# Kernel tuning notes

Measured on AMD Instinct MI355X. Metric: run time of the kernel, lower is better.

Reference implementation:

```python
import jax, jax.numpy as jnp
import numpy as np

GAMMA = 0.3
R_PERCENT = 0.2
LAMBDA_PENALTY = 0.5
EPS = 1e-06

B_SZ, N_HEADS, K_FULL = 16, 32, 32768
K_IMG = 16384


def _zscore(x):
    mu = x.mean(axis=-1, keepdims=True)
    std = jnp.sqrt(((x - mu) ** 2).mean(axis=-1, keepdims=True))  # unbiased=False
    return (x - mu) / (std + EPS)


def _topk_binary(scores, k):
    # scores: [B,H] -> binary mask [B,H]; only strictly-positive topk values count
    vals, idx = jax.lax.top_k(scores, k)
    b = jnp.arange(scores.shape[0])[:, None]
    return jnp.zeros_like(scores).at[b, idx].set((vals > 0).astype(scores.dtype))


def setup_inputs() -> dict:
    key = jax.random.key(0)
    k1, k2, k3, k4, k5 = jax.random.split(key, 5)
    attn_logits_last = jax.random.normal(k1, (B_SZ, N_HEADS, K_FULL), dtype=jnp.float32)
    # exactly K_IMG image tokens per row (alternating pattern -> strided gather)
    image_mask = jnp.tile((jnp.arange(K_FULL) % 2 == 0).astype(jnp.int32)[None, :], (B_SZ, 1))
    feat_C = jax.random.normal(k2, (B_SZ, K_IMG), dtype=jnp.float32)
    feat_A = jax.random.normal(k3, (B_SZ, K_IMG), dtype=jnp.float32)
    feat_D = jax.random.normal(k4, (B_SZ, K_IMG), dtype=jnp.float32)
    feat_B = jax.random.normal(k5, (B_SZ, K_IMG), dtype=jnp.float32)
    return {"attn_logits_last": attn_logits_last, "image_mask": image_mask,
            "feat_C": feat_C, "feat_A": feat_A, "feat_D": feat_D, "feat_B": feat_B}


def reference(attn_logits_last, image_mask, feat_C, feat_A, feat_D, feat_B):
    B, H, K_full = attn_logits_last.shape
    K_img = feat_C.shape[1]

    # --- compute_rf ---
    C_t = jax.nn.relu(_zscore(feat_C))
    A_t = jax.nn.sigmoid(_zscore(feat_A))
    D_t = jax.nn.sigmoid(_zscore(feat_D))
    B_t = jax.nn.sigmoid(_zscore(feat_B))
    denom = jnp.maximum(1.0 + LAMBDA_PENALTY * (D_t + B_t), EPS)
    rf = jnp.maximum(C_t * A_t / denom, 0.0)  # [B,K_img]

    # --- align: positions of image tokens (exactly K_img ones per row) ---
    idx = jax.vmap(lambda m: jnp.nonzero(m, size=K_img)[0])(image_mask)  # [B,K_img]

    # --- image-normalized attention ---
    probs_full = jax.nn.softmax(attn_logits_last, axis=-1)
    mask_f = image_mask[:, None, :].astype(attn_logits_last.dtype)  # [B,1,K_full]
    probs_img = probs_full * mask_f
    probs_img_norm = probs_img / jnp.maximum(probs_img.sum(axis=-1, keepdims=True), EPS)
    attn_img_norm = jnp.take_along_axis(probs_img_norm, idx[:, None, :], axis=-1)  # [B,H,K_img]

    # --- dynamic head roles ---
    low_rf = jnp.maximum(1.0 - rf, 0.0)
    s_pos = (attn_img_norm * rf[:, None, :]).sum(axis=-1)   # [B,H]
    s_neg = (attn_img_norm * low_rf[:, None, :]).sum(axis=-1)
    k_heads = min(max(1, int(np.ceil(R_PERCENT * H))), H)
    m_pos = _topk_binary(s_pos, k_heads)
    neg_scores = jnp.where(m_pos > 0, -jnp.inf, s_neg)
    m_neg = _topk_binary(neg_scores, k_heads) * (m_pos == 0).astype(s_pos.dtype)

    # --- delta and scatter back to full logits ---
    delta_img = GAMMA * (m_pos[:, :, None] * rf[:, None, :]
                         - m_neg[:, :, None] * low_rf[:, None, :])  # [B,H,K_img]
    delta_full = jax.vmap(
        lambda d, i: jnp.zeros((H, K_full), attn_logits_last.dtype).at[:, i].set(d)
    )(delta_img, idx)
    delta_full = delta_full * mask_f
    return attn_logits_last + delta_full
```

## Files before the change

kernel.cpp:

```cpp
#include <hip/hip_runtime.h>
#include <math.h>

#define GAMMA 0.3f
#define EPS 1e-6f
#define B_SZ 16
#define NH 32
#define KF 32768
#define KI 16384
#define KHEADS 7

constexpr int OFF_MU    = 0;
constexpr int OFF_SD    = 64;
constexpr int OFF_RAWS  = 128;
constexpr int OFF_RAWP  = 640;
constexpr int OFF_RAWN  = 1152;
constexpr int IOFF_BSUM = 1664;
constexpr int OFF_RF    = 4096;
constexpr int OFF_RFF   = OFF_RF + B_SZ * KI;

__global__ __launch_bounds__(256) void k_stats_cnt(const float* __restrict__ fC,
        const float* __restrict__ fA, const float* __restrict__ fD,
        const float* __restrict__ fB, const int* __restrict__ mask,
        float* __restrict__ ws) {
    __shared__ double r1[256], r2[256];
    __shared__ int sred[256];
    int bid = blockIdx.x, t = threadIdx.x;
    if (bid < 64) {
        int b = bid >> 2, f = bid & 3;
        const float* src;
        if (f == 0) src = fC; else if (f == 1) src = fA; else if (f == 2) src = fD; else src = fB;
        src += (size_t)b * KI;
        double s = 0.0, s2 = 0.0;
        for (int i = t; i < KI / 4; i += 256) {
            float4 v = ((const float4*)src)[i];
            s  += (double)v.x + (double)v.y + (double)v.z + (double)v.w;
            s2 += (double)v.x * v.x + (double)v.y * v.y + (double)v.z * v.z + (double)v.w * v.w;
        }
        r1[t] = s; r2[t] = s2; __syncthreads();
        for (int off = 128; off > 0; off >>= 1) {
            if (t < off) { r1[t] += r1[t + off]; r2[t] += r2[t + off]; }
            __syncthreads();
        }
        if (t == 0) {
            double mu  = r1[0] * (1.0 / KI);
            double var = fmax(r2[0] * (1.0 / KI) - mu * mu, 0.0);
            ws[OFF_MU + bid] = (float)mu;
            ws[OFF_SD + bid] = (float)(sqrt(var) + (double)EPS);
        }
    } else {
        int cblk = bid - 64;
        if (cblk < 6) ws[OFF_RAWS + cblk * 256 + t] = 0.f;
        const int* mrow = mask + (size_t)cblk * 2048;
        int4 m0 = *(const int4*)(mrow + t * 8);
        int4 m1 = *(const int4*)(mrow + t * 8 + 4);
        int cnt = (m0.x != 0) + (m0.y != 0) + (m0.z != 0) + (m0.w != 0)
                + (m1.x != 0) + (m1.y != 0) + (m1.z != 0) + (m1.w != 0);
        sred[t] = cnt; __syncthreads();
        for (int off = 128; off > 0; off >>= 1) {
            if (t < off) sred[t] += sred[t + off];
            __syncthreads();
        }
        if (t == 0) ((int*)ws)[IOFF_BSUM + cblk] = sred[0];
    }
}

__global__ __launch_bounds__(256) void k_rf(const float* __restrict__ fC,
        const float* __restrict__ fA, const float* __restrict__ fD,
        const float* __restrict__ fB, float* __restrict__ ws) {
    int blk = blockIdx.x, t = threadIdx.x;
    int base = blk * 1024 + t * 4;
    int b = base >> 14;
    const float* mu = ws + OFF_MU + b * 4;
    const float* sd = ws + OFF_SD + b * 4;
    float4 vC = *(const float4*)(fC + base);
    float4 vA = *(const float4*)(fA + base);
    float4 vD = *(const float4*)(fD + base);
    float4 vB = *(const float4*)(fB + base);
    float rf4[4];
    float c4[4] = {vC.x, vC.y, vC.z, vC.w};
    float a4[4] = {vA.x, vA.y, vA.z, vA.w};
    float d4[4] = {vD.x, vD.y, vD.z, vD.w};
    float b4[4] = {vB.x, vB.y, vB.z, vB.w};
    #pragma unroll
    for (int j = 0; j < 4; ++j) {
        float Ct = fmaxf((c4[j] - mu[0]) / sd[0], 0.f);
        float At = 1.f / (1.f + __expf(-((a4[j] - mu[1]) / sd[1])));
        float Dt = 1.f / (1.f + __expf(-((d4[j] - mu[2]) / sd[2])));
        float Bt = 1.f / (1.f + __expf(-((b4[j] - mu[3]) / sd[3])));
        float denom = fmaxf(1.f + 0.5f * (Dt + Bt), EPS);
        rf4[j] = fmaxf(Ct * At / denom, 0.f);
    }
    *(float4*)(ws + OFF_RF + base) = *(float4*)rf4;
}

__global__ __launch_bounds__(256) void k_expand(const int* __restrict__ mask,
                                                float* __restrict__ ws) {
    int blk = blockIdx.x, t = threadIdx.x;
    int b = blk >> 4, c = blk & 15;
    const int* bsum = (const int*)ws + IOFF_BSUM;
    int boff = 0;
    for (int i = 0; i < c; ++i) boff += bsum[(b << 4) + i];
    const int* mrow = mask + (size_t)blk * 2048;
    int4 m0 = *(const int4*)(mrow + t * 8);
    int4 m1 = *(const int4*)(mrow + t * 8 + 4);
    int mv[8] = {m0.x, m0.y, m0.z, m0.w, m1.x, m1.y, m1.z, m1.w};
    int cnt = 0;
    #pragma unroll
    for (int j = 0; j < 8; ++j) cnt += (mv[j] != 0);
    __shared__ int sc[256];
    sc[t] = cnt; __syncthreads();
    for (int off = 1; off < 256; off <<= 1) {
        int v = (t >= off) ? sc[t - off] : 0;
        __syncthreads();
        sc[t] += v;
        __syncthreads();
    }
    int r = boff + sc[t] - cnt;
    const float* rf = ws + OFF_RF + b * KI;
    float vr[8];
    #pragma unroll
    for (int j = 0; j < 8; ++j) {
        if (mv[j]) { vr[j] = rf[r]; ++r; }
        else       { vr[j] = -1.f; }
    }
    float* rff = ws + OFF_RFF + (size_t)blk * 2048 + t * 8;
    *(float4*)(rff)     = *(float4*)(vr);
    *(float4*)(rff + 4) = *(float4*)(vr + 4);
}

__global__ __launch_bounds__(256) void k_scores(const float* __restrict__ attn,
                                                float* __restrict__ ws) {
    int g = blockIdx.x, t = threadIdx.x;
    int bh = g >> 1, half = g & 1;
    int b = bh >> 5;
    const float* xr  = attn + ((size_t)bh << 15) + ((size_t)half << 14);
    const float* rff = ws + OFF_RFF + ((size_t)b << 15) + ((size_t)half << 14);
    float S = 0.f, P = 0.f, N = 0.f;
    #pragma unroll 4
    for (int i = 0; i < 16; ++i) {
        int k = (i * 256 + t) * 4;
        float4 xs = *(const float4*)(xr + k);
        float4 rv = *(const float4*)(rff + k);
        float xa[4] = {xs.x, xs.y, xs.z, xs.w};
        float va[4] = {rv.x, rv.y, rv.z, rv.w};
        #pragma unroll
        for (int j = 0; j < 4; ++j) {
            float e = __expf(xa[j]);
            bool on = va[j] >= 0.f;
            float rfv  = fmaxf(va[j], 0.f);
            float lrfv = on ? fmaxf(1.f - va[j], 0.f) : 0.f;
            S += on ? e : 0.f;
            P = fmaf(e, rfv, P);
            N = fmaf(e, lrfv, N);
        }
    }
    __shared__ float rs[256], rp[256], rn[256];
    rs[t] = S; rp[t] = P; rn[t] = N;
    __syncthreads();
    for (int off = 128; off > 0; off >>= 1) {
        if (t < off) { rs[t] += rs[t + off]; rp[t] += rp[t + off]; rn[t] += rn[t + off]; }
        __syncthreads();
    }
    if (t == 0) {
        atomicAdd(&ws[OFF_RAWS + bh], rs[0]);
        atomicAdd(&ws[OFF_RAWP + bh], rp[0]);
        atomicAdd(&ws[OFF_RAWN + bh], rn[0]);
    }
}

__global__ __launch_bounds__(256) void k_out(const float* __restrict__ attn,
        const float* __restrict__ ws, float* __restrict__ out) {
    unsigned int t = threadIdx.x;
    unsigned int flat = (blockIdx.x * 256 + t) * 4;
    unsigned int bh = flat >> 15;
    unsigned int b  = bh >> 5;
    unsigned int h  = bh & 31;

    __shared__ float ssp[NH], snv[NH];
    __shared__ int smp[NH];
    __shared__ float s_gp, s_gn;
    if (t < NH) {
        float S0 = ws[OFF_RAWS + b * NH + t];
        ssp[t] = ws[OFF_RAWP + b * NH + t] / S0;
        snv[t] = ws[OFF_RAWN + b * NH + t] / S0;
    }
    __syncthreads();
    if (t < NH) {
        float sp = ssp[t];
        int cnt = 0;
        for (int j = 0; j < NH; ++j) { float o = ssp[j]; cnt += (o > sp) || (o == sp && (int)j < (int)t); }
        smp[t] = (cnt < KHEADS) && (sp > 0.f);
    }
    __syncthreads();
    if (t < NH && smp[t]) snv[t] = -INFINITY;
    __syncthreads();
    if (t == 0) {
        float gp = 0.f, gn = 0.f;
        if (smp[h]) gp = GAMMA;
        else {
            float nv = snv[h];
            int cnt = 0;
            for (int j = 0; j < NH; ++j) { float o = snv[j]; cnt += (o > nv) || (o == nv && j < (int)h); }
            if ((cnt < KHEADS) && (nv > 0.f)) gn = GAMMA;
        }
        s_gp = gp; s_gn = gn;
    }
    __syncthreads();

    float gp = s_gp, gn = s_gn;
    const float* rff = ws + OFF_RFF + ((size_t)b << 15);
    unsigned int k = flat & (KF - 1);
    float4 xs = *(const float4*)(attn + flat);
    float4 rv = *(const float4*)(rff + k);
    float va[4] = {rv.x, rv.y, rv.z, rv.w};
    float xa[4] = {xs.x, xs.y, xs.z, xs.w};
    float oa[4];
    #pragma unroll
    for (int j = 0; j < 4; ++j) {
        bool on = va[j] >= 0.f;
        float rfv  = fmaxf(va[j], 0.f);
        float lrfv = on ? fmaxf(1.f - va[j], 0.f) : 0.f;
        oa[j] = xa[j] + gp * rfv - gn * lrfv;
    }
    float4 o = {oa[0], oa[1], oa[2], oa[3]};
    *(float4*)(out + flat) = o;
}

extern "C" void kernel_launch(void* const* d_in, const int* in_sizes, int n_in,
                              void* d_out, int out_size, void* d_ws, size_t ws_size,
                              hipStream_t stream) {
    const float* attn = (const float*)d_in[0];
    const int*   mask = (const int*)d_in[1];
    const float* fC   = (const float*)d_in[2];
    const float* fA   = (const float*)d_in[3];
    const float* fD   = (const float*)d_in[4];
    const float* fB   = (const float*)d_in[5];
    float* out = (float*)d_out;
    float* ws = (float*)d_ws;

    k_stats_cnt<<<320, 256, 0, stream>>>(fC, fA, fD, fB, mask, ws);
    k_rf       <<<256, 256, 0, stream>>>(fC, fA, fD, fB, ws);
    k_expand   <<<256, 256, 0, stream>>>(mask, ws);
    k_scores   <<<1024, 256, 0, stream>>>(attn, ws);
    k_out      <<<(B_SZ * NH * KF / 4) / 256, 256, 0, stream>>>(attn, ws, out);
}
```

Baseline: 154.0 us.

## Fuse rf into expand and fuse scores+output via cooperative grid sync

The rf computation is merged into the expand kernel, which computes rf values for its chunk into shared memory and no longer writes an intermediate rf array. The scores and output kernels are fused into one cooperative kernel of 1024 blocks that reduces head scores, does a grid-wide sync, then writes the output from the same attention rows, which it can hope to find still in cache. This removes two launches and part of the re-read of the attention tensor. The risk is that grid.sync and co-residency limits make the launch fail, in which case the code falls back to the original two kernels.

Result: slower. 290.3 us (+88.5%).

```diff
diff --git a/kernel.cpp b/kernel.cpp
--- a/kernel.cpp
+++ b/kernel.cpp
@@ -1,5 +1,8 @@
 #include <hip/hip_runtime.h>
+#include <hip/hip_cooperative_groups.h>
 #include <math.h>
+
+namespace cg = cooperative_groups;
 
 #define GAMMA 0.3f
 #define EPS 1e-6f
@@ -15,8 +18,7 @@
 constexpr int OFF_RAWP  = 640;
 constexpr int OFF_RAWN  = 1152;
 constexpr int IOFF_BSUM = 1664;
-constexpr int OFF_RF    = 4096;
-constexpr int OFF_RFF   = OFF_RF + B_SZ * KI;
+constexpr int OFF_RFF   = 4096;
 
 __global__ __launch_bounds__(256) void k_stats_cnt(const float* __restrict__ fC,
         const float* __restrict__ fA, const float* __restrict__ fD,
@@ -64,37 +66,12 @@
     }
 }
 
-__global__ __launch_bounds__(256) void k_rf(const float* __restrict__ fC,
+__global__ __launch_bounds__(256) void k_rf_expand(const float* __restrict__ fC,
         const float* __restrict__ fA, const float* __restrict__ fD,
-        const float* __restrict__ fB, float* __restrict__ ws) {
-    int blk = blockIdx.x, t = threadIdx.x;
-    int base = blk * 1024 + t * 4;
-    int b = base >> 14;
-    const float* mu = ws + OFF_MU + b * 4;
-    const float* sd = ws + OFF_SD + b * 4;
-    float4 vC = *(const float4*)(fC + base);
-    float4 vA = *(const float4*)(fA + base);
-    float4 vD = *(const float4*)(fD + base);
-    float4 vB = *(const float4*)(fB + base);
-    float rf4[4];
-    float c4[4] = {vC.x, vC.y, vC.z, vC.w};
-    float a4[4] = {vA.x, vA.y, vA.z, vA.w};
-    float d4[4] = {vD.x, vD.y, vD.z, vD.w};
-    float b4[4] = {vB.x, vB.y, vB.z, vB.w};
-    #pragma unroll
-    for (int j = 0; j < 4; ++j) {
-        float Ct = fmaxf((c4[j] - mu[0]) / sd[0], 0.f);
-        float At = 1.f / (1.f + __expf(-((a4[j] - mu[1]) / sd[1])));
-        float Dt = 1.f / (1.f + __expf(-((d4[j] - mu[2]) / sd[2])));
-        float Bt = 1.f / (1.f + __expf(-((b4[j] - mu[3]) / sd[3])));
-        float denom = fmaxf(1.f + 0.5f * (Dt + Bt), EPS);
-        rf4[j] = fmaxf(Ct * At / denom, 0.f);
-    }
-    *(float4*)(ws + OFF_RF + base) = *(float4*)rf4;
-}
-
-__global__ __launch_bounds__(256) void k_expand(const int* __restrict__ mask,
-                                                float* __restrict__ ws) {
+        const float* __restrict__ fB, const int* __restrict__ mask,
+        float* __restrict__ ws) {
+    __shared__ int sc[256];
+    __shared__ float rfbuf[2048];
     int blk = blockIdx.x, t = threadIdx.x;
     int b = blk >> 4, c = blk & 15;
     const int* bsum = (const int*)ws + IOFF_BSUM;
@@ -107,7 +84,6 @@
     int cnt = 0;
     #pragma unroll
     for (int j = 0; j < 8; ++j) cnt += (mv[j] != 0);
-    __shared__ int sc[256];
     sc[t] = cnt; __syncthreads();
     for (int off = 1; off < 256; off <<= 1) {
         int v = (t >= off) ? sc[t - off] : 0;
@@ -115,12 +91,26 @@
         sc[t] += v;
         __syncthreads();
     }
-    int r = boff + sc[t] - cnt;
-    const float* rf = ws + OFF_RF + b * KI;
+    int total = sc[255];
+    int rloc = sc[t] - cnt;
+    float mu0 = ws[OFF_MU + b * 4 + 0], sd0 = ws[OFF_SD + b * 4 + 0];
+    float mu1 = ws[OFF_MU + b * 4 + 1], sd1 = ws[OFF_SD + b * 4 + 1];
+    float mu2 = ws[OFF_MU + b * 4 + 2], sd2 = ws[OFF_SD + b * 4 + 2];
+    float mu3 = ws[OFF_MU + b * 4 + 3], sd3 = ws[OFF_SD + b * 4 + 3];
+    for (int j = t; j < total; j += 256) {
+        size_t idx = (size_t)b * KI + boff + j;
+        float Ct = fmaxf((fC[idx] - mu0) / sd0, 0.f);
+        float At = 1.f / (1.f + __expf(-((fA[idx] - mu1) / sd1)));
+        float Dt = 1.f / (1.f + __expf(-((fD[idx] - mu2) / sd2)));
+        float Bt = 1.f / (1.f + __expf(-((fB[idx] - mu3) / sd3)));
+        float denom = fmaxf(1.f + 0.5f * (Dt + Bt), EPS);
+        rfbuf[j] = fmaxf(Ct * At / denom, 0.f);
+    }
+    __syncthreads();
     float vr[8];
     #pragma unroll
     for (int j = 0; j < 8; ++j) {
-        if (mv[j]) { vr[j] = rf[r]; ++r; }
+        if (mv[j]) { vr[j] = rfbuf[rloc]; ++rloc; }
         else       { vr[j] = -1.f; }
     }
     float* rff = ws + OFF_RFF + (size_t)blk * 2048 + t * 8;
@@ -128,14 +118,8 @@
     *(float4*)(rff + 4) = *(float4*)(vr + 4);
 }
 
-__global__ __launch_bounds__(256) void k_scores(const float* __restrict__ attn,
-                                                float* __restrict__ ws) {
-    int g = blockIdx.x, t = threadIdx.x;
-    int bh = g >> 1, half = g & 1;
-    int b = bh >> 5;
-    const float* xr  = attn + ((size_t)bh << 15) + ((size_t)half << 14);
-    const float* rff = ws + OFF_RFF + ((size_t)b << 15) + ((size_t)half << 14);
-    float S = 0.f, P = 0.f, N = 0.f;
+__device__ __forceinline__ void score_accum(const float* __restrict__ xr,
+        const float* __restrict__ rff, int t, float& S, float& P, float& N) {
     #pragma unroll 4
     for (int i = 0; i < 16; ++i) {
         int k = (i * 256 + t) * 4;
@@ -154,28 +138,10 @@
             N = fmaf(e, lrfv, N);
         }
     }
-    __shared__ float rs[256], rp[256], rn[256];
-    rs[t] = S; rp[t] = P; rn[t] = N;
-    __syncthreads();
-    for (int off = 128; off > 0; off >>= 1) {
-        if (t < off) { rs[t] += rs[t + off]; rp[t] += rp[t + off]; rn[t] += rn[t + off]; }
-        __syncthreads();
-    }
-    if (t == 0) {
-        atomicAdd(&ws[OFF_RAWS + bh], rs[0]);
-        atomicAdd(&ws[OFF_RAWP + bh], rp[0]);
-        atomicAdd(&ws[OFF_RAWN + bh], rn[0]);
-    }
-}
-
-__global__ __launch_bounds__(256) void k_out(const float* __restrict__ attn,
-        const float* __restrict__ ws, float* __restrict__ out) {
-    unsigned int t = threadIdx.x;
-    unsigned int flat = (blockIdx.x * 256 + t) * 4;
-    unsigned int bh = flat >> 15;
-    unsigned int b  = bh >> 5;
-    unsigned int h  = bh & 31;
-
+}
+
+__device__ __forceinline__ void topk_gains(const float* __restrict__ ws,
+        unsigned int b, unsigned int h, unsigned int t, float* gp_out, float* gn_out) {
     __shared__ float ssp[NH], snv[NH];
     __shared__ int smp[NH];
     __shared__ float s_gp, s_gn;
@@ -188,7 +154,7 @@
     if (t < NH) {
         float sp = ssp[t];
         int cnt = 0;
-        for (int j = 0; j < NH; ++j) { float o = ssp[j]; cnt += (o > sp) || (o == sp && (int)j < (int)t); }
+        for (int j = 0; j < NH; ++j) { float o = ssp[j]; cnt += (o > sp) || (o == sp && j < (int)t); }
         smp[t] = (cnt < KHEADS) && (sp > 0.f);
     }
     __syncthreads();
@@ -206,8 +172,93 @@
         s_gp = gp; s_gn = gn;
     }
     __syncthreads();
-
-    float gp = s_gp, gn = s_gn;
+    *gp_out = s_gp; *gn_out = s_gn;
+}
+
+__global__ __launch_bounds__(256) void k_fused(const float* __restrict__ attn,
+        float* __restrict__ ws, float* __restrict__ out) {
+    cg::grid_group grid = cg::this_grid();
+    int g = blockIdx.x, t = threadIdx.x;
+    int bh = g >> 1, half = g & 1;
+    unsigned int b = bh >> 5, h = bh & 31;
+    size_t abase = ((size_t)bh << 15) + ((size_t)half << 14);
+    size_t rbase = ((size_t)b  << 15) + ((size_t)half << 14);
+    const float* xr  = attn + abase;
+    const float* rff = ws + OFF_RFF + rbase;
+
+    float S = 0.f, P = 0.f, N = 0.f;
+    score_accum(xr, rff, t, S, P, N);
+    __shared__ float rs[256], rp[256], rn[256];
+    rs[t] = S; rp[t] = P; rn[t] = N;
+    __syncthreads();
+    for (int off = 128; off > 0; off >>= 1) {
+        if (t < off) { rs[t] += rs[t + off]; rp[t] += rp[t + off]; rn[t] += rn[t + off]; }
+        __syncthreads();
+    }
+    if (t == 0) {
+        atomicAdd(&ws[OFF_RAWS + bh], rs[0]);
+        atomicAdd(&ws[OFF_RAWP + bh], rp[0]);
+        atomicAdd(&ws[OFF_RAWN + bh], rn[0]);
+    }
+
+    grid.sync();
+
+    float gp, gn;
+    topk_gains(ws, b, h, t, &gp, &gn);
+
+    float* orow = out + abase;
+    #pragma unroll 4
+    for (int i = 0; i < 16; ++i) {
+        int k = (i * 256 + t) * 4;
+        float4 xs = *(const float4*)(xr + k);
+        float4 rv = *(const float4*)(rff + k);
+        float xa[4] = {xs.x, xs.y, xs.z, xs.w};
+        float va[4] = {rv.x, rv.y, rv.z, rv.w};
+        float oa[4];
+        #pragma unroll
+        for (int j = 0; j < 4; ++j) {
+            bool on = va[j] >= 0.f;
+            float rfv  = fmaxf(va[j], 0.f);
+            float lrfv = on ? fmaxf(1.f - va[j], 0.f) : 0.f;
+            oa[j] = xa[j] + gp * rfv - gn * lrfv;
+        }
+        float4 o = {oa[0], oa[1], oa[2], oa[3]};
+        *(float4*)(orow + k) = o;
+    }
+}
+
+__global__ __launch_bounds__(256) void k_scores(const float* __restrict__ attn,
+                                                float* __restrict__ ws) {
+    int g = blockIdx.x, t = threadIdx.x;
+    int bh = g >> 1, half = g & 1;
+    int b = bh >> 5;
+    const float* xr  = attn + ((size_t)bh << 15) + ((size_t)half << 14);
+    const float* rff = ws + OFF_RFF + ((size_t)b << 15) + ((size_t)half << 14);
+    float S = 0.f, P = 0.f, N = 0.f;
+    score_accum(xr, rff, t, S, P, N);
+    __shared__ float rs[256], rp[256], rn[256];
+    rs[t] = S; rp[t] = P; rn[t] = N;
+    __syncthreads();
+    for (int off = 128; off > 0; off >>= 1) {
+        if (t < off) { rs[t] += rs[t + off]; rp[t] += rp[t + off]; rn[t] += rn[t + off]; }
+        __syncthreads();
+    }
+    if (t == 0) {
+        atomicAdd(&ws[OFF_RAWS + bh], rs[0]);
+        atomicAdd(&ws[OFF_RAWP + bh], rp[0]);
+        atomicAdd(&ws[OFF_RAWN + bh], rn[0]);
+    }
+}
+
+__global__ __launch_bounds__(256) void k_out(const float* __restrict__ attn,
+        const float* __restrict__ ws, float* __restrict__ out) {
+    unsigned int t = threadIdx.x;
+    unsigned int flat = (blockIdx.x * 256 + t) * 4;
+    unsigned int bh = flat >> 15;
+    unsigned int b  = bh >> 5;
+    unsigned int h  = bh & 31;
+    float gp, gn;
+    topk_gains(ws, b, h, t, &gp, &gn);
     const float* rff = ws + OFF_RFF + ((size_t)b << 15);
     unsigned int k = flat & (KF - 1);
     float4 xs = *(const float4*)(attn + flat);
@@ -239,8 +290,14 @@
     float* ws = (float*)d_ws;
 
     k_stats_cnt<<<320, 256, 0, stream>>>(fC, fA, fD, fB, mask, ws);
-    k_rf       <<<256, 256, 0, stream>>>(fC, fA, fD, fB, ws);
-    k_expand   <<<256, 256, 0, stream>>>(mask, ws);
-    k_scores   <<<1024, 256, 0, stream>>>(attn, ws);
-    k_out      <<<(B_SZ * NH * KF / 4) / 256, 256, 0, stream>>>(attn, ws, out);
-}
+    k_rf_expand<<<256, 256, 0, stream>>>(fC, fA, fD, fB, mask, ws);
+
+    void* args[] = {(void*)&attn, (void*)&ws, (void*)&out};
+    hipError_t e = hipLaunchCooperativeKernel((void*)k_fused, dim3(1024), dim3(256),
+                                              args, 0, stream);
+    if (e != hipSuccess) {
+        (void)hipGetLastError();
+        k_scores<<<1024, 256, 0, stream>>>(attn, ws);
+        k_out<<<(B_SZ * NH * KF / 4) / 256, 256, 0, stream>>>(attn, ws, out);
+    }
+}
```
